# Optimization experiments

Measured on AMD Instinct MI355X. Metric: run time of the kernel, lower is better.

Reference implementation:

```python
import jax, jax.numpy as jnp
import numpy as np

B_, L, DM = 4, 1024, 1024
DI, DS, DR, DC = 1024, 16, 64, 4
NH = 4
DK = DM // NH


def setup_inputs() -> dict:
    key = jax.random.key(0)
    ks = jax.random.split(key, 16)
    def w(i, shape, scale=0.02):
        return jax.random.normal(ks[i], shape, dtype=jnp.float32) * scale
    inp = {
        "x": jax.random.normal(ks[0], (B_, L, DM), dtype=jnp.float32),
        "xx": jax.random.normal(ks[1], (B_, L, DI), dtype=jnp.float32),
        "in_proj_w": w(2, (DI, DM)),
        "conv_w": w(3, (DI, 1, DC)),            # depthwise conv, groups=DI
        "conv_b": jnp.zeros((DI,), jnp.float32),
        "x_proj_w": w(4, (DR + 2 * DS, DI)),
        "dt_proj_w": w(5, (DI, DR)),
        "dt_proj_b": jnp.zeros((DI,), jnp.float32),
        "A_log": jnp.log(jnp.tile(jnp.arange(1, DS + 1, dtype=jnp.float32)[None, :], (DI, 1))),
        "D": jnp.ones((DI,), jnp.float32),
        "wq": w(6, (DM, DM)), "bq": jnp.zeros((DM,), jnp.float32),
        "wk": w(7, (DM, DM)), "bk": jnp.zeros((DM,), jnp.float32),
        "wv": w(8, (DM, DM)), "bv": jnp.zeros((DM,), jnp.float32),
        "wo": w(9, (DM, DM)), "bo": jnp.zeros((DM,), jnp.float32),
    }
    return inp


def _stim_forward(x, xx, in_proj_w, conv_w, conv_b, x_proj_w, dt_proj_w, dt_proj_b,
                  A_log, D, wq, bq, wk, bk, wv, bv, wo, bo):
    b, l, _ = xx.shape
    # query branch: in_proj (Linear, no bias)
    q = x @ in_proj_w.T                                    # (b, l, DI)
    # kv branch: causal depthwise conv1d (padding d_conv-1, truncated to l)
    xc = jnp.transpose(xx, (0, 2, 1))                      # (b, DI, l)
    xc = jax.lax.conv_general_dilated(
        xc, conv_w, window_strides=(1,), padding=[(DC - 1, 0)],
        dimension_numbers=("NCH", "OIH", "NCH"), feature_group_count=DI)
    xc = xc + conv_b[None, :, None]
    u = jax.nn.silu(jnp.transpose(xc, (0, 2, 1)))          # (b, l, DI)
    # SSM parameter projections
    A = -jnp.exp(A_log)                                    # (DI, DS)
    x_dbl = u @ x_proj_w.T                                 # (b, l, DR+2*DS)
    delta, Bm, Cm = jnp.split(x_dbl, [DR, DR + DS], axis=-1)
    delta = jax.nn.softplus(delta @ dt_proj_w.T + dt_proj_b)  # (b, l, DI)
    deltaA = jnp.exp(jnp.einsum("bld,dn->bldn", delta, A))    # (b, l, DI, DS)
    deltaBu = jnp.einsum("bld,bln,bld->bldn", delta, Bm, u)   # (b, l, DI, DS)
    # selective scan over time
    def step(h, inp):
        dA_t, dBu_t, C_t = inp
        h = dA_t * h + dBu_t                               # (b, DI, DS)
        y_t = jnp.einsum("bdn,bn->bd", h, C_t)             # (b, DI)
        return h, y_t
    h0 = jnp.zeros((b, DI, DS), dtype=u.dtype)
    _, ys = jax.lax.scan(step, h0, (jnp.moveaxis(deltaA, 1, 0),
                                    jnp.moveaxis(deltaBu, 1, 0),
                                    jnp.moveaxis(Cm, 1, 0)))
    y = jnp.moveaxis(ys, 0, 1) + u * D                     # (b, l, DI)
    # cross attention: query = q, key/value = y
    Q = (q @ wq.T + bq).reshape(b, l, NH, DK).transpose(0, 2, 1, 3)
    K = (y @ wk.T + bk).reshape(b, l, NH, DK).transpose(0, 2, 1, 3)
    V = (y @ wv.T + bv).reshape(b, l, NH, DK).transpose(0, 2, 1, 3)
    scale = 1.0 / np.sqrt(DK).astype(np.float32)
    scores = jnp.einsum("bhqd,bhkd->bhqk", Q, K) * scale
    attn = jax.nn.softmax(scores, axis=-1)
    out = jnp.einsum("bhqk,bhkd->bhqd", attn, V)
    out = out.transpose(0, 2, 1, 3).reshape(b, l, DM)
    return out @ wo.T + bo


def reference(x, xx, in_proj_w, conv_w, conv_b, x_proj_w, dt_proj_w, dt_proj_b,
              A_log, D, wq, bq, wk, bk, wv, bv, wo, bo):
    return _stim_forward(x, xx, in_proj_w, conv_w, conv_b, x_proj_w, dt_proj_w,
                         dt_proj_b, A_log, D, wq, bq, wk, bk, wv, bv, wo, bo)
```

## Files before the change

kernel.cpp:

```cpp
#include <hip/hip_runtime.h>
#include <math.h>

#define B_  4
#define L_  1024
#define DM  1024
#define DI  1024
#define DS  16
#define DR  64
#define DCV 4
#define NH  4
#define DK  256

#define NCH 32
#define CHL (L_ / NCH)

typedef __attribute__((ext_vector_type(8))) short short8;
typedef __attribute__((ext_vector_type(4))) float floatx4;

static __device__ __forceinline__ unsigned short f2bf(float f) {
    unsigned int u = __float_as_uint(f);
    u += 0x7fffu + ((u >> 16) & 1u);
    return (unsigned short)(u >> 16);
}
static __device__ __forceinline__ float bf2f(unsigned short s) {
    return __uint_as_float(((unsigned int)s) << 16);
}

#define GLL(gp, lp) __builtin_amdgcn_global_load_lds( \
        (const __attribute__((address_space(1))) void*)(gp), \
        (__attribute__((address_space(3))) void*)(lp), 16, 0, 0)

static __device__ __forceinline__ void xcd_rect(int gx, int gy, int& tx, int& ty)
{
    int n = blockIdx.x + gx * blockIdx.y;
    if ((gx & 1) == 0 && (gy & 3) == 0) {
        int xcd = n & 7, j = n >> 3;
        int hx = gx >> 1, qy = gy >> 2;
        tx = (xcd & 1) * hx + (j % hx);
        ty = (xcd >> 1) * qy + (j / hx);
    } else {
        tx = blockIdx.x; ty = blockIdx.y;
    }
}

struct PrepArgs {
    const float* xx; const float* cw; const float* cb;
    unsigned short* ub;
    const float* xs; unsigned short* xd;
    const float* s[6]; unsigned short* d[6];
    int n[6];
    int ns[6];
    const float* tsrc; unsigned short* tdst;
};

__global__ __launch_bounds__(256) void prep(PrepArgs pa)
{
    __shared__ unsigned short tl[32][36];
    int bid = blockIdx.x, tid = threadIdx.x;
    if (bid < 16384) {
        int idx = bid * 256 + tid;
        int d = idx & (DI - 1);
        int l = (idx >> 10) & (L_ - 1);
        int b = idx >> 20;
        const float* xb = pa.xx + (size_t)b * L_ * DI + d;
        float z = pa.cb[d];
#pragma unroll
        for (int j = 0; j < DCV; j++) {
            int t = l - (DCV - 1) + j;
            if (t >= 0) z += xb[(size_t)t * DI] * pa.cw[d * DCV + j];
        }
        float v = z / (1.0f + __expf(-z));
        pa.ub[idx] = f2bf(v);
        return;
    }
    bid -= 16384;
    if (bid < 4096) {
        int i = (bid * 256 + tid) * 4;
        float4 v = *(const float4*)(pa.xs + i);
        ushort4 o;
        o.x = f2bf(v.x); o.y = f2bf(v.y); o.z = f2bf(v.z); o.w = f2bf(v.w);
        *(ushort4*)(pa.xd + i) = o;
        return;
    }
    bid -= 4096;
#pragma unroll
    for (int r = 0; r < 6; r++) {
        int nb = pa.n[r] >> 10;
        if (bid < nb) {
            int i = (bid * 256 + tid) * 4;
            int ns = pa.ns[r];
            const float* s = pa.s[r];
            ushort4 o;
            if (i + 4 <= ns) {
                float4 v = *(const float4*)(s + i);
                o.x = f2bf(v.x); o.y = f2bf(v.y); o.z = f2bf(v.z); o.w = f2bf(v.w);
            } else {
                float v[4];
#pragma unroll
                for (int j = 0; j < 4; j++) v[j] = (i + j < ns) ? s[i + j] : 0.f;
                o.x = f2bf(v[0]); o.y = f2bf(v[1]); o.z = f2bf(v[2]); o.w = f2bf(v[3]);
            }
            *(ushort4*)(pa.d[r] + i) = o;
            return;
        }
        bid -= nb;
    }
    int j0 = (bid >> 5) * 32;
    int n0 = (bid & 31) * 32;
    int r = tid >> 3, c4 = (tid & 7) * 4;
    float4 v = *(const float4*)(pa.tsrc + (size_t)(j0 + r) * 1024 + n0 + c4);
    tl[r][c4 + 0] = f2bf(v.x); tl[r][c4 + 1] = f2bf(v.y);
    tl[r][c4 + 2] = f2bf(v.z); tl[r][c4 + 3] = f2bf(v.w);
    __syncthreads();
    ushort4 o;
    o.x = tl[c4 + 0][r]; o.y = tl[c4 + 1][r];
    o.z = tl[c4 + 2][r]; o.w = tl[c4 + 3][r];
    *(ushort4*)(pa.tdst + (size_t)(n0 + r) * 1024 + j0 + c4) = o;
}

struct GDesc {
    const unsigned short* A;
    const unsigned short* W;
    const float* bias;
    float* Cf;
    unsigned short* Cb;
    int K, lda, ldw, ldc, ldc2;
    int mode;
    float scale;
    int gx, gy;
};
struct GArgs { GDesc g[3]; };

__global__ __launch_bounds__(256) void gemm_multi(GArgs ga)
{
    GDesc g = ga.g[blockIdx.z];
    int bx, by;
    xcd_rect(gridDim.x, gridDim.y, bx, by);
    if (bx >= g.gx || by >= g.gy) return;

    __shared__ __align__(16) unsigned short Asm[3][128 * 32];
    __shared__ __align__(16) unsigned short Bsm[3][128 * 32];

    int tid = threadIdx.x;
    int wid = tid >> 6;
    int lane = tid & 63;
    int wm = wid & 1, wn = wid >> 1;
    int lr = lane & 15, quad = lane >> 4;
    int sq = quad ^ ((lr >> 1) & 3);

    const unsigned short* Ab = g.A + (size_t)by * 128 * g.lda;
    const unsigned short* Wb = g.W + (size_t)bx * 128 * g.ldw;

    int srow = tid >> 2;
    int scol = ((tid & 3) ^ ((tid >> 3) & 3)) * 8;
    const unsigned short* Ap = Ab + (size_t)srow * g.lda + scol;
    const unsigned short* Wp = Wb + (size_t)srow * g.ldw + scol;

    int lbase = (wid * 16) * 32;

    floatx4 acc[4][4];
#pragma unroll
    for (int i = 0; i < 4; i++)
#pragma unroll
        for (int j = 0; j < 4; j++) acc[i][j] = (floatx4){0.f, 0.f, 0.f, 0.f};

#define STAGE_M(buf) do { \
        GLL(Ap, &Asm[buf][lbase]); \
        GLL(Ap + (size_t)64 * g.lda, &Asm[buf][lbase + 64 * 32]); \
        GLL(Wp, &Bsm[buf][lbase]); \
        GLL(Wp + (size_t)64 * g.ldw, &Bsm[buf][lbase + 64 * 32]); \
        Ap += 32; Wp += 32; \
    } while (0)

    int nK = g.K >> 5;
    STAGE_M(0);
    if (nK > 1) STAGE_M(1);

    int cur = 0, stg = 2;
    for (int k = 0; k < nK - 1; k++) {
        asm volatile("s_waitcnt vmcnt(4)" ::: "memory");
        __builtin_amdgcn_s_barrier();
        __builtin_amdgcn_sched_barrier(0);

        short8 af[4], bf[4];
#pragma unroll
        for (int mt = 0; mt < 4; mt++)
            af[mt] = *(const short8*)&Asm[cur][(wm * 64 + mt * 16 + lr) * 32 + sq * 8];
#pragma unroll
        for (int nt = 0; nt < 4; nt++)
            bf[nt] = *(const short8*)&Bsm[cur][(wn * 64 + nt * 16 + lr) * 32 + sq * 8];

        if (k + 2 < nK) {
            STAGE_M(stg);
            stg = (stg == 2) ? 0 : stg + 1;
        }

        __builtin_amdgcn_s_setprio(1);
#pragma unroll
        for (int mt = 0; mt < 4; mt++)
#pragma unroll
            for (int nt = 0; nt < 4; nt++)
                acc[mt][nt] = __builtin_amdgcn_mfma_f32_16x16x32_bf16(
                    af[mt], bf[nt], acc[mt][nt], 0, 0, 0);
        __builtin_amdgcn_s_setprio(0);
        cur = (cur == 2) ? 0 : cur + 1;
    }
    {
        asm volatile("s_waitcnt vmcnt(0)" ::: "memory");
        __builtin_amdgcn_s_barrier();
        __builtin_amdgcn_sched_barrier(0);

        short8 af[4], bf[4];
#pragma unroll
        for (int mt = 0; mt < 4; mt++)
            af[mt] = *(const short8*)&Asm[cur][(wm * 64 + mt * 16 + lr) * 32 + sq * 8];
#pragma unroll
        for (int nt = 0; nt < 4; nt++)
            bf[nt] = *(const short8*)&Bsm[cur][(wn * 64 + nt * 16 + lr) * 32 + sq * 8];
        __builtin_amdgcn_s_setprio(1);
#pragma unroll
        for (int mt = 0; mt < 4; mt++)
#pragma unroll
            for (int nt = 0; nt < 4; nt++)
                acc[mt][nt] = __builtin_amdgcn_mfma_f32_16x16x32_bf16(
                    af[mt], bf[nt], acc[mt][nt], 0, 0, 0);
        __builtin_amdgcn_s_setprio(0);
    }
#undef STAGE_M

    int bm = by * 128, bn = bx * 128;
    int m = g.mode & 3;
#pragma unroll
    for (int mt = 0; mt < 4; mt++) {
#pragma unroll
        for (int nt = 0; nt < 4; nt++) {
            int row0 = bm + wm * 64 + mt * 16 + quad * 4;
            int col = bn + wn * 64 + nt * 16 + lr;
            float bv = g.bias ? g.bias[col] : 0.f;
#pragma unroll
            for (int i = 0; i < 4; i++) {
                float v = acc[mt][nt][i] * g.scale + bv;
                if (g.mode & 4) v = (v > 15.f) ? v : log1pf(__expf(v));
                if (m == 0) {
                    g.Cf[(size_t)(row0 + i) * g.ldc + col] = v;
                } else if (m == 1) {
                    g.Cb[(size_t)(row0 + i) * g.ldc + col] = f2bf(v);
                } else {
                    g.Cf[(size_t)(row0 + i) * g.ldc + col] = v;
                    g.Cb[(size_t)(row0 + i) * g.ldc2 + col] = f2bf(v);
                }
            }
        }
    }
}

__global__ __launch_bounds__(256) void gemm_multi64(GArgs ga)
{
    GDesc g = ga.g[blockIdx.z];
    int bx, by;
    xcd_rect(gridDim.x, gridDim.y, bx, by);
    if (bx >= g.gx || by >= g.gy) return;

    __shared__ __align__(16) unsigned short Asm[3][64 * 32];
    __shared__ __align__(16) unsigned short Bsm[3][128 * 32];

    int tid = threadIdx.x;
    int wid = tid >> 6;
    int lane = tid & 63;
    int wm = wid & 1, wn = wid >> 1;
    int lr = lane & 15, quad = lane >> 4;
    int sq = quad ^ ((lr >> 1) & 3);

    const unsigned short* Ab = g.A + (size_t)by * 64 * g.lda;
    const unsigned short* Wb = g.W + (size_t)bx * 128 * g.ldw;

    int srow = tid >> 2;
    int scol = ((tid & 3) ^ ((tid >> 3) & 3)) * 8;
    const unsigned short* Ap = Ab + (size_t)srow * g.lda + scol;
    const unsigned short* Wp = Wb + (size_t)srow * g.ldw + scol;

    int lbase = (wid * 16) * 32;

    floatx4 acc[2][4];
#pragma unroll
    for (int i = 0; i < 2; i++)
#pragma unroll
        for (int j = 0; j < 4; j++) acc[i][j] = (floatx4){0.f, 0.f, 0.f, 0.f};

#define STAGE_S(buf) do { \
        GLL(Ap, &Asm[buf][lbase]); \
        GLL(Wp, &Bsm[buf][lbase]); \
        GLL(Wp + (size_t)64 * g.ldw, &Bsm[buf][lbase + 64 * 32]); \
        Ap += 32; Wp += 32; \
    } while (0)

    int nK = g.K >> 5;
    STAGE_S(0);
    if (nK > 1) STAGE_S(1);

    int cur = 0, stg = 2;
    for (int k = 0; k < nK - 1; k++) {
        asm volatile("s_waitcnt vmcnt(3)" ::: "memory");
        __builtin_amdgcn_s_barrier();
        __builtin_amdgcn_sched_barrier(0);

        short8 af[2], bf[4];
#pragma unroll
        for (int mt = 0; mt < 2; mt++)
            af[mt] = *(const short8*)&Asm[cur][(wm * 32 + mt * 16 + lr) * 32 + sq * 8];
#pragma unroll
        for (int nt = 0; nt < 4; nt++)
            bf[nt] = *(const short8*)&Bsm[cur][(wn * 64 + nt * 16 + lr) * 32 + sq * 8];

        if (k + 2 < nK) {
            STAGE_S(stg);
            stg = (stg == 2) ? 0 : stg + 1;
        }

        __builtin_amdgcn_s_setprio(1);
#pragma unroll
        for (int mt = 0; mt < 2; mt++)
#pragma unroll
            for (int nt = 0; nt < 4; nt++)
                acc[mt][nt] = __builtin_amdgcn_mfma_f32_16x16x32_bf16(
                    af[mt], bf[nt], acc[mt][nt], 0, 0, 0);
        __builtin_amdgcn_s_setprio(0);
        cur = (cur == 2) ? 0 : cur + 1;
    }
    {
        asm volatile("s_waitcnt vmcnt(0)" ::: "memory");
        __builtin_amdgcn_s_barrier();
        __builtin_amdgcn_sched_barrier(0);

        short8 af[2], bf[4];
#pragma unroll
        for (int mt = 0; mt < 2; mt++)
            af[mt] = *(const short8*)&Asm[cur][(wm * 32 + mt * 16 + lr) * 32 + sq * 8];
#pragma unroll
        for (int nt = 0; nt < 4; nt++)
            bf[nt] = *(const short8*)&Bsm[cur][(wn * 64 + nt * 16 + lr) * 32 + sq * 8];
        __builtin_amdgcn_s_setprio(1);
#pragma unroll
        for (int mt = 0; mt < 2; mt++)
#pragma unroll
            for (int nt = 0; nt < 4; nt++)
                acc[mt][nt] = __builtin_amdgcn_mfma_f32_16x16x32_bf16(
                    af[mt], bf[nt], acc[mt][nt], 0, 0, 0);
        __builtin_amdgcn_s_setprio(0);
    }
#undef STAGE_S

    int bm = by * 64, bn = bx * 128;
    int m = g.mode & 3;
#pragma unroll
    for (int mt = 0; mt < 2; mt++) {
#pragma unroll
        for (int nt = 0; nt < 4; nt++) {
            int row0 = bm + wm * 32 + mt * 16 + quad * 4;
            int col = bn + wn * 64 + nt * 16 + lr;
            float bv = g.bias ? g.bias[col] : 0.f;
#pragma unroll
            for (int i = 0; i < 4; i++) {
                float v = acc[mt][nt][i] * g.scale + bv;
                if (g.mode & 4) v = (v > 15.f) ? v : log1pf(__expf(v));
                if (m == 0) {
                    g.Cf[(size_t)(row0 + i) * g.ldc + col] = v;
                } else if (m == 1) {
                    g.Cb[(size_t)(row0 + i) * g.ldc + col] = f2bf(v);
                } else {
                    g.Cf[(size_t)(row0 + i) * g.ldc + col] = v;
                    g.Cb[(size_t)(row0 + i) * g.ldc2 + col] = f2bf(v);
                }
            }
        }
    }
}

__global__ __launch_bounds__(256) void gemm_batched(
    const unsigned short* __restrict__ A, const unsigned short* __restrict__ W,
    unsigned short* __restrict__ C,
    int K, int lda, int ldw, int ldc,
    long long sA1, long long sA2, long long sW1, long long sW2,
    long long sC1, long long sC2, float scale)
{
    __shared__ __align__(16) unsigned short Asm[3][128 * 32];
    __shared__ __align__(16) unsigned short Bsm[3][128 * 32];

    int bx, by;
    xcd_rect(gridDim.x, gridDim.y, bx, by);

    int z = blockIdx.z;
    long long bq = z >> 2, hq = z & 3;
    int tid = threadIdx.x;
    int wid = tid >> 6;
    int lane = tid & 63;
    int wm = wid & 1, wn = wid >> 1;
    int lr = lane & 15, quad = lane >> 4;
    int sq = quad ^ ((lr >> 1) & 3);

    const unsigned short* Ab = A + bq * sA1 + hq * sA2 + (size_t)by * 128 * lda;
    const unsigned short* Wb = W + bq * sW1 + hq * sW2 + (size_t)bx * 128 * ldw;

    int srow = tid >> 2;
    int scol = ((tid & 3) ^ ((tid >> 3) & 3)) * 8;
    const unsigned short* Ap = Ab + (size_t)srow * lda + scol;
    const unsigned short* Wp = Wb + (size_t)srow * ldw + scol;

    int lbase = (wid * 16) * 32;

    floatx4 acc[4][4];
#pragma unroll
    for (int i = 0; i < 4; i++)
#pragma unroll
        for (int j = 0; j < 4; j++) acc[i][j] = (floatx4){0.f, 0.f, 0.f, 0.f};

#define STAGE_B(buf) do { \
        GLL(Ap, &Asm[buf][lbase]); \
        GLL(Ap + (size_t)64 * lda, &Asm[buf][lbase + 64 * 32]); \
        GLL(Wp, &Bsm[buf][lbase]); \
        GLL(Wp + (size_t)64 * ldw, &Bsm[buf][lbase + 64 * 32]); \
        Ap += 32; Wp += 32; \
    } while (0)

    int nK = K >> 5;
    STAGE_B(0);
    if (nK > 1) STAGE_B(1);

    int cur = 0, stg = 2;
    for (int k = 0; k < nK - 1; k++) {
        asm volatile("s_waitcnt vmcnt(4)" ::: "memory");
        __builtin_amdgcn_s_barrier();
        __builtin_amdgcn_sched_barrier(0);

        short8 af[4], bf[4];
#pragma unroll
        for (int mt = 0; mt < 4; mt++)
            af[mt] = *(const short8*)&Asm[cur][(wm * 64 + mt * 16 + lr) * 32 + sq * 8];
#pragma unroll
        for (int nt = 0; nt < 4; nt++)
            bf[nt] = *(const short8*)&Bsm[cur][(wn * 64 + nt * 16 + lr) * 32 + sq * 8];

        if (k + 2 < nK) {
            STAGE_B(stg);
            stg = (stg == 2) ? 0 : stg + 1;
        }

        __builtin_amdgcn_s_setprio(1);
#pragma unroll
        for (int mt = 0; mt < 4; mt++)
#pragma unroll
            for (int nt = 0; nt < 4; nt++)
                acc[mt][nt] = __builtin_amdgcn_mfma_f32_16x16x32_bf16(
                    af[mt], bf[nt], acc[mt][nt], 0, 0, 0);
        __builtin_amdgcn_s_setprio(0);
        cur = (cur == 2) ? 0 : cur + 1;
    }
    {
        asm volatile("s_waitcnt vmcnt(0)" ::: "memory");
        __builtin_amdgcn_s_barrier();
        __builtin_amdgcn_sched_barrier(0);

        short8 af[4], bf[4];
#pragma unroll
        for (int mt = 0; mt < 4; mt++)
            af[mt] = *(const short8*)&Asm[cur][(wm * 64 + mt * 16 + lr) * 32 + sq * 8];
#pragma unroll
        for (int nt = 0; nt < 4; nt++)
            bf[nt] = *(const short8*)&Bsm[cur][(wn * 64 + nt * 16 + lr) * 32 + sq * 8];
        __builtin_amdgcn_s_setprio(1);
#pragma unroll
        for (int mt = 0; mt < 4; mt++)
#pragma unroll
            for (int nt = 0; nt < 4; nt++)
                acc[mt][nt] = __builtin_amdgcn_mfma_f32_16x16x32_bf16(
                    af[mt], bf[nt], acc[mt][nt], 0, 0, 0);
        __builtin_amdgcn_s_setprio(0);
    }
#undef STAGE_B

    long long coff = bq * sC1 + hq * sC2;
    int bm = by * 128, bn = bx * 128;
    unsigned short* Cb = C + coff;

#pragma unroll
    for (int mt = 0; mt < 4; mt++) {
#pragma unroll
        for (int nt = 0; nt < 4; nt++) {
            int row0 = bm + wm * 64 + mt * 16 + quad * 4;
            int col = bn + wn * 64 + nt * 16 + lr;
#pragma unroll
            for (int i = 0; i < 4; i++)
                Cb[(size_t)(row0 + i) * ldc + col] = f2bf(acc[mt][nt][i] * scale);
        }
    }
}

__global__ __launch_bounds__(256) void gemm_batched64(
    const unsigned short* __restrict__ A, const unsigned short* __restrict__ W,
    unsigned short* __restrict__ C,
    int K, int lda, int ldw, int ldc,
    long long sA1, long long sA2, long long sW1, long long sW2,
    long long sC1, long long sC2, float scale)
{
    __shared__ __align__(16) unsigned short Asm[3][64 * 32];
    __shared__ __align__(16) unsigned short Bsm[3][128 * 32];

    int bx, by;
    xcd_rect(gridDim.x, gridDim.y, bx, by);

    int z = blockIdx.z;
    long long bq = z >> 2, hq = z & 3;
    int tid = threadIdx.x;
    int wid = tid >> 6;
    int lane = tid & 63;
    int wm = wid & 1, wn = wid >> 1;
    int lr = lane & 15, quad = lane >> 4;
    int sq = quad ^ ((lr >> 1) & 3);

    const unsigned short* Ab = A + bq * sA1 + hq * sA2 + (size_t)by * 64 * lda;
    const unsigned short* Wb = W + bq * sW1 + hq * sW2 + (size_t)bx * 128 * ldw;

    int srow = tid >> 2;
    int scol = ((tid & 3) ^ ((tid >> 3) & 3)) * 8;
    const unsigned short* Ap = Ab + (size_t)srow * lda + scol;
    const unsigned short* Wp = Wb + (size_t)srow * ldw + scol;

    int lbase = (wid * 16) * 32;

    floatx4 acc[2][4];
#pragma unroll
    for (int i = 0; i < 2; i++)
#pragma unroll
        for (int j = 0; j < 4; j++) acc[i][j] = (floatx4){0.f, 0.f, 0.f, 0.f};

#define STAGE_S(buf) do { \
        GLL(Ap, &Asm[buf][lbase]); \
        GLL(Wp, &Bsm[buf][lbase]); \
        GLL(Wp + (size_t)64 * ldw, &Bsm[buf][lbase + 64 * 32]); \
        Ap += 32; Wp += 32; \
    } while (0)

    int nK = K >> 5;
    STAGE_S(0);
    if (nK > 1) STAGE_S(1);

    int cur = 0, stg = 2;
    for (int k = 0; k < nK - 1; k++) {
        asm volatile("s_waitcnt vmcnt(3)" ::: "memory");
        __builtin_amdgcn_s_barrier();
        __builtin_amdgcn_sched_barrier(0);

        short8 af[2], bf[4];
#pragma unroll
        for (int mt = 0; mt < 2; mt++)
            af[mt] = *(const short8*)&Asm[cur][(wm * 32 + mt * 16 + lr) * 32 + sq * 8];
#pragma unroll
        for (int nt = 0; nt < 4; nt++)
            bf[nt] = *(const short8*)&Bsm[cur][(wn * 64 + nt * 16 + lr) * 32 + sq * 8];

        if (k + 2 < nK) {
            STAGE_S(stg);
            stg = (stg == 2) ? 0 : stg + 1;
        }

        __builtin_amdgcn_s_setprio(1);
#pragma unroll
        for (int mt = 0; mt < 2; mt++)
#pragma unroll
            for (int nt = 0; nt < 4; nt++)
                acc[mt][nt] = __builtin_amdgcn_mfma_f32_16x16x32_bf16(
                    af[mt], bf[nt], acc[mt][nt], 0, 0, 0);
        __builtin_amdgcn_s_setprio(0);
        cur = (cur == 2) ? 0 : cur + 1;
    }
    {
        asm volatile("s_waitcnt vmcnt(0)" ::: "memory");
        __builtin_amdgcn_s_barrier();
        __builtin_amdgcn_sched_barrier(0);

        short8 af[2], bf[4];
#pragma unroll
        for (int mt = 0; mt < 2; mt++)
            af[mt] = *(const short8*)&Asm[cur][(wm * 32 + mt * 16 + lr) * 32 + sq * 8];
#pragma unroll
        for (int nt = 0; nt < 4; nt++)
            bf[nt] = *(const short8*)&Bsm[cur][(wn * 64 + nt * 16 + lr) * 32 + sq * 8];
        __builtin_amdgcn_s_setprio(1);
#pragma unroll
        for (int mt = 0; mt < 2; mt++)
#pragma unroll
            for (int nt = 0; nt < 4; nt++)
                acc[mt][nt] = __builtin_amdgcn_mfma_f32_16x16x32_bf16(
                    af[mt], bf[nt], acc[mt][nt], 0, 0, 0);
        __builtin_amdgcn_s_setprio(0);
    }
#undef STAGE_S

    long long coff = bq * sC1 + hq * sC2;
    int bm = by * 64, bn = bx * 128;
    unsigned short* Cb = C + coff;

#pragma unroll
    for (int mt = 0; mt < 2; mt++) {
#pragma unroll
        for (int nt = 0; nt < 4; nt++) {
            int row0 = bm + wm * 32 + mt * 16 + quad * 4;
            int col = bn + wn * 64 + nt * 16 + lr;
#pragma unroll
            for (int i = 0; i < 4; i++)
                Cb[(size_t)(row0 + i) * ldc + col] = f2bf(acc[mt][nt][i] * scale);
        }
    }
}

__global__ __launch_bounds__(256) void scan_a(
    const float* __restrict__ delta, const unsigned short* __restrict__ u,
    const float* __restrict__ xdbl, const float* __restrict__ A_log,
    float* __restrict__ Hc, float* __restrict__ sumdv)
{
    int gid = blockIdx.x * 256 + threadIdx.x;
    int c = gid >> 12;
    int bd = gid & 4095;
    int b = bd >> 10, d = bd & 1023;

    float a[16];
#pragma unroll
    for (int j = 0; j < 4; j++) {
        float4 al = *(const float4*)(A_log + d * 16 + j * 4);
        a[j * 4 + 0] = -__expf(al.x); a[j * 4 + 1] = -__expf(al.y);
        a[j * 4 + 2] = -__expf(al.z); a[j * 4 + 3] = -__expf(al.w);
    }
    float h[16];
#pragma unroll
    for (int n = 0; n < 16; n++) h[n] = 0.f;
    float sd = 0.f;

    int t0 = c * CHL;
    const float* dp = delta + ((size_t)(b * L_) + t0) * DI + d;
    const unsigned short* up = u + ((size_t)(b * L_) + t0) * DI + d;
    const float* xp = xdbl + ((size_t)(b * L_) + t0) * 128;

#pragma unroll 4
    for (int t = 0; t < CHL; t++) {
        float dv = dp[t * DI];
        float uv = bf2f(up[t * DI]);
        float duv = dv * uv;
        sd += dv;
        float Bv[16];
#pragma unroll
        for (int j = 0; j < 4; j++) {
            float4 bq = *(const float4*)(xp + t * 128 + 64 + j * 4);
            Bv[j * 4 + 0] = bq.x; Bv[j * 4 + 1] = bq.y;
            Bv[j * 4 + 2] = bq.z; Bv[j * 4 + 3] = bq.w;
        }
#pragma unroll
        for (int n = 0; n < 16; n++)
            h[n] = __expf(dv * a[n]) * h[n] + duv * Bv[n];
    }

    float* hp = Hc + ((size_t)c * 4096 + bd) * 16;
#pragma unroll
    for (int j = 0; j < 4; j++)
        *(float4*)(hp + j * 4) = make_float4(h[j * 4], h[j * 4 + 1], h[j * 4 + 2], h[j * 4 + 3]);
    sumdv[c * 4096 + bd] = sd;
}

__global__ __launch_bounds__(256) void scan_b(
    float* __restrict__ Hc, const float* __restrict__ sumdv,
    const float* __restrict__ A_log)
{
    int bd = blockIdx.x * 256 + threadIdx.x;
    int d = bd & 1023;

    float a[16];
#pragma unroll
    for (int j = 0; j < 4; j++) {
        float4 al = *(const float4*)(A_log + d * 16 + j * 4);
        a[j * 4 + 0] = -__expf(al.x); a[j * 4 + 1] = -__expf(al.y);
        a[j * 4 + 2] = -__expf(al.z); a[j * 4 + 3] = -__expf(al.w);
    }
    float H[16];
#pragma unroll
    for (int n = 0; n < 16; n++) H[n] = 0.f;

    for (int c = 0; c < NCH; c++) {
        float* hp = Hc + ((size_t)c * 4096 + bd) * 16;
        float sdv = sumdv[c * 4096 + bd];
        float hc[16];
#pragma unroll
        for (int j = 0; j < 4; j++) {
            float4 q = *(const float4*)(hp + j * 4);
            hc[j * 4 + 0] = q.x; hc[j * 4 + 1] = q.y; hc[j * 4 + 2] = q.z; hc[j * 4 + 3] = q.w;
        }
#pragma unroll
        for (int j = 0; j < 4; j++)
            *(float4*)(hp + j * 4) = make_float4(H[j * 4], H[j * 4 + 1], H[j * 4 + 2], H[j * 4 + 3]);
#pragma unroll
        for (int n = 0; n < 16; n++)
            H[n] = __expf(a[n] * sdv) * H[n] + hc[n];
    }
}

__global__ __launch_bounds__(256) void scan_c(
    const float* __restrict__ delta, const unsigned short* __restrict__ u,
    const float* __restrict__ xdbl, const float* __restrict__ A_log,
    const float* __restrict__ Dv, const float* __restrict__ Hstart,
    unsigned short* __restrict__ y)
{
    int gid = blockIdx.x * 256 + threadIdx.x;
    int c = gid >> 12;
    int bd = gid & 4095;
    int b = bd >> 10, d = bd & 1023;

    float a[16];
#pragma unroll
    for (int j = 0; j < 4; j++) {
        float4 al = *(const float4*)(A_log + d * 16 + j * 4);
        a[j * 4 + 0] = -__expf(al.x); a[j * 4 + 1] = -__expf(al.y);
        a[j * 4 + 2] = -__expf(al.z); a[j * 4 + 3] = -__expf(al.w);
    }
    float h[16];
    const float* hp = Hstart + ((size_t)c * 4096 + bd) * 16;
#pragma unroll
    for (int j = 0; j < 4; j++) {
        float4 q = *(const float4*)(hp + j * 4);
        h[j * 4 + 0] = q.x; h[j * 4 + 1] = q.y; h[j * 4 + 2] = q.z; h[j * 4 + 3] = q.w;
    }
    float Dd = Dv[d];

    int t0 = c * CHL;
    const float* dp = delta + ((size_t)(b * L_) + t0) * DI + d;
    const unsigned short* up = u + ((size_t)(b * L_) + t0) * DI + d;
    const float* xp = xdbl + ((size_t)(b * L_) + t0) * 128;
    unsigned short* yp = y + ((size_t)(b * L_) + t0) * DI + d;

#pragma unroll 4
    for (int t = 0; t < CHL; t++) {
        float dv = dp[t * DI];
        float uv = bf2f(up[t * DI]);
        float duv = dv * uv;
        float Bv[16], Cv[16];
#pragma unroll
        for (int j = 0; j < 4; j++) {
            float4 bq = *(const float4*)(xp + t * 128 + 64 + j * 4);
            Bv[j * 4 + 0] = bq.x; Bv[j * 4 + 1] = bq.y;
            Bv[j * 4 + 2] = bq.z; Bv[j * 4 + 3] = bq.w;
            float4 cq = *(const float4*)(xp + t * 128 + 80 + j * 4);
            Cv[j * 4 + 0] = cq.x; Cv[j * 4 + 1] = cq.y;
            Cv[j * 4 + 2] = cq.z; Cv[j * 4 + 3] = cq.w;
        }
        float ys = 0.f;
#pragma unroll
        for (int n = 0; n < 16; n++) {
            h[n] = __expf(dv * a[n]) * h[n] + duv * Bv[n];
            ys += h[n] * Cv[n];
        }
        yp[t * DI] = f2bf(ys + uv * Dd);
    }
}

__global__ __launch_bounds__(256) void softmax_transpose(
    unsigned short* __restrict__ S,
    const unsigned short* __restrict__ V, unsigned short* __restrict__ VT)
{
    __shared__ unsigned short tl[32][36];
    int bid = blockIdx.x;
    if (bid < 4096) {
        int row = bid * 4 + (threadIdx.x >> 6);
        int lane = threadIdx.x & 63;
        unsigned short* p = S + (size_t)row * 1024;

        float v[16];
#pragma unroll
        for (int ch = 0; ch < 4; ch++) {
            ushort4 u4 = *(const ushort4*)(p + ch * 256 + lane * 4);
            v[ch * 4 + 0] = bf2f(u4.x); v[ch * 4 + 1] = bf2f(u4.y);
            v[ch * 4 + 2] = bf2f(u4.z); v[ch * 4 + 3] = bf2f(u4.w);
        }
        float m = -1e30f;
#pragma unroll
        for (int i = 0; i < 16; i++) m = fmaxf(m, v[i]);
#pragma unroll
        for (int off = 32; off >= 1; off >>= 1) m = fmaxf(m, __shfl_xor(m, off));
        float s = 0.f;
#pragma unroll
        for (int i = 0; i < 16; i++) { v[i] = __expf(v[i] - m); s += v[i]; }
#pragma unroll
        for (int off = 32; off >= 1; off >>= 1) s += __shfl_xor(s, off);
        float inv = 1.0f / s;
#pragma unroll
        for (int ch = 0; ch < 4; ch++) {
            ushort4 o;
            o.x = f2bf(v[ch * 4 + 0] * inv); o.y = f2bf(v[ch * 4 + 1] * inv);
            o.z = f2bf(v[ch * 4 + 2] * inv); o.w = f2bf(v[ch * 4 + 3] * inv);
            *(ushort4*)(p + ch * 256 + lane * 4) = o;
        }
        return;
    }
    int tb = bid - 4096;
    int bh = tb >> 8;
    int rem = tb & 255;
    int d0 = (rem >> 5) * 32;
    int l0 = (rem & 31) * 32;
    int b = bh >> 2, h = bh & 3;
    int tid = threadIdx.x;
    int r = tid >> 3, c4 = (tid & 7) * 4;

    const unsigned short* src = V + ((size_t)(b * L_ + l0 + r)) * 1024 + h * DK + d0 + c4;
    ushort4 v = *(const ushort4*)src;
    tl[r][c4 + 0] = v.x; tl[r][c4 + 1] = v.y; tl[r][c4 + 2] = v.z; tl[r][c4 + 3] = v.w;
    __syncthreads();

    unsigned short* dst = VT + ((size_t)bh * DK + d0 + r) * L_ + l0 + c4;
    ushort4 o;
    o.x = tl[c4 + 0][r]; o.y = tl[c4 + 1][r]; o.z = tl[c4 + 2][r]; o.w = tl[c4 + 3][r];
    *(ushort4*)dst = o;
}

extern "C" void kernel_launch(void* const* d_in, const int* in_sizes, int n_in,
                              void* d_out, int out_size, void* d_ws, size_t ws_size,
                              hipStream_t stream)
{
    const float* x         = (const float*)d_in[0];
    const float* xx        = (const float*)d_in[1];
    const float* in_proj_w = (const float*)d_in[2];
    const float* conv_w    = (const float*)d_in[3];
    const float* conv_b    = (const float*)d_in[4];
    const float* x_proj_w  = (const float*)d_in[5];
    const float* dt_proj_w = (const float*)d_in[6];
    const float* dt_proj_b = (const float*)d_in[7];
    const float* A_log     = (const float*)d_in[8];
    const float* Dvec      = (const float*)d_in[9];
    const float* wq        = (const float*)d_in[10];
    const float* bq        = (const float*)d_in[11];
    const float* wk        = (const float*)d_in[12];
    const float* bk        = (const float*)d_in[13];
    const float* wv        = (const float*)d_in[14];
    const float* bv        = (const float*)d_in[15];
    const float* wo        = (const float*)d_in[16];
    const float* bo        = (const float*)d_in[17];
    float* out = (float*)d_out;

    char* w = (char*)d_ws;
    const size_t MB = 1024 * 1024, KB = 1024;
    float*          Hc     = (float*)(w + 0);
    float*          delta  = (float*)(w + 16 * MB);
    unsigned short* Sbuf   = (unsigned short*)(w + 0);
    unsigned short* x_bf   = (unsigned short*)(w + 32 * MB);
    unsigned short* Q_bf   = (unsigned short*)(w + 40 * MB);
    unsigned short* VT     = Q_bf;
    unsigned short* y_bf   = (unsigned short*)(w + 48 * MB);
    unsigned short* AO     = y_bf;
    unsigned short* K_bf   = (unsigned short*)(w + 56 * MB);
    unsigned short* V_bf   = (unsigned short*)(w + 64 * MB);
    unsigned short* u_bf   = (unsigned short*)(w + 72 * MB);
    float*          xdbl   = (float*)(w + 80 * MB);
    unsigned short* xdblb  = (unsigned short*)(w + 82 * MB);
    unsigned short* w_inT  = (unsigned short*)(w + 83 * MB);
    unsigned short* w_q    = (unsigned short*)(w + 85 * MB);
    unsigned short* w_k    = (unsigned short*)(w + 87 * MB);
    unsigned short* w_v    = (unsigned short*)(w + 89 * MB);
    unsigned short* w_o    = (unsigned short*)(w + 91 * MB);
    unsigned short* w_xp   = (unsigned short*)(w + 93 * MB);
    unsigned short* w_dt   = (unsigned short*)(w + 93 * MB + 256 * KB);
    float*          sumdv  = (float*)(w + 93 * MB + 384 * KB);
    unsigned short* W_qin  = (unsigned short*)(w + 95 * MB);

    dim3 blk(256);
    const long long LL = L_;

    PrepArgs pa;
    pa.xx = xx; pa.cw = conv_w; pa.cb = conv_b; pa.ub = u_bf;
    pa.xs = x; pa.xd = x_bf;
    pa.s[0] = wq;        pa.d[0] = w_q;  pa.n[0] = 1048576; pa.ns[0] = 1048576;
    pa.s[1] = wk;        pa.d[1] = w_k;  pa.n[1] = 1048576; pa.ns[1] = 1048576;
    pa.s[2] = wv;        pa.d[2] = w_v;  pa.n[2] = 1048576; pa.ns[2] = 1048576;
    pa.s[3] = wo;        pa.d[3] = w_o;  pa.n[3] = 1048576; pa.ns[3] = 1048576;
    pa.s[4] = x_proj_w;  pa.d[4] = w_xp; pa.n[4] = 131072;  pa.ns[4] = 98304;
    pa.s[5] = dt_proj_w; pa.d[5] = w_dt; pa.n[5] = 65536;   pa.ns[5] = 65536;
    pa.tsrc = in_proj_w; pa.tdst = w_inT;
    prep<<<dim3(25792), blk, 0, stream>>>(pa);

    {
        GArgs ga = {};
        ga.g[0] = (GDesc){w_q, w_inT, nullptr, nullptr, W_qin,
                          1024, 1024, 1024, 1024, 0, 1, 1.0f, 8, 16};
        ga.g[1] = (GDesc){u_bf, w_xp, nullptr, xdbl, xdblb,
                          1024, 1024, 1024, 128, 128, 2, 1.0f, 1, 64};
        gemm_multi64<<<dim3(8, 64, 2), blk, 0, stream>>>(ga);
    }
    {
        GArgs ga = {};
        ga.g[0] = (GDesc){xdblb, w_dt, dt_proj_b, delta, nullptr,
                          64, 128, 64, 1024, 0, 0 | 4, 1.0f, 8, 64};
        gemm_multi64<<<dim3(8, 64, 1), blk, 0, stream>>>(ga);
    }
    scan_a<<<dim3(512), blk, 0, stream>>>(delta, u_bf, xdbl, A_log, Hc, sumdv);
    scan_b<<<dim3(16), blk, 0, stream>>>(Hc, sumdv, A_log);
    scan_c<<<dim3(512), blk, 0, stream>>>(delta, u_bf, xdbl, A_log, Dvec, Hc, y_bf);

    {
        GArgs ga = {};
        ga.g[0] = (GDesc){x_bf, W_qin, bq, nullptr, Q_bf, 1024, 1024, 1024, 1024, 0, 1, 1.0f, 8, 32};
        ga.g[1] = (GDesc){y_bf, w_k, bk, nullptr, K_bf, 1024, 1024, 1024, 1024, 0, 1, 1.0f, 8, 32};
        ga.g[2] = (GDesc){y_bf, w_v, bv, nullptr, V_bf, 1024, 1024, 1024, 1024, 0, 1, 1.0f, 8, 32};
        gemm_multi<<<dim3(8, 32, 3), blk, 0, stream>>>(ga);
    }
    gemm_batched<<<dim3(8, 8, 16), blk, 0, stream>>>(Q_bf, K_bf, Sbuf,
        DK, 1024, 1024, 1024,
        LL * 1024, 256, LL * 1024, 256,
        4 * LL * 1024, LL * 1024, 0.0625f);
    softmax_transpose<<<dim3(8192), blk, 0, stream>>>(Sbuf, V_bf, VT);
    gemm_batched64<<<dim3(2, 16, 16), blk, 0, stream>>>(Sbuf, VT, AO,
        1024, 1024, 1024, 1024,
        4 * LL * 1024, LL * 1024,
        4 * (long long)DK * 1024, (long long)DK * 1024,
        LL * 1024, 256, 1.0f);
    {
        GArgs ga = {};
        ga.g[0] = (GDesc){AO, w_o, bo, out, nullptr, 1024, 1024, 1024, 1024, 0, 0, 1.0f, 8, 64};
        gemm_multi64<<<dim3(8, 64, 1), blk, 0, stream>>>(ga);
    }
}
```

Measured before the change: 388.1 us.

## Fuse softmax into PV GEMM prologue and A-fragment load path

Removes the standalone softmax pass over the score matrix. Each PV GEMM block now computes its rows' max and sum-of-exp in a prologue by reading the 64 score rows directly, then applies exp and normalization to the A fragments right before the MFMAs. The V transpose becomes its own kernel. This saves a full read-write of the 16M-element score buffer, but every PV block redundantly rereads its score rows (two grid columns share them), and exp work is added inside the MFMA loop.

```diff
diff --git a/kernel.cpp b/kernel.cpp
--- a/kernel.cpp
+++ b/kernel.cpp
@@ -495,7 +495,7 @@
     }
 }
 
-__global__ __launch_bounds__(256) void gemm_batched64(
+__global__ __launch_bounds__(256) void gemm_pv64(
     const unsigned short* __restrict__ A, const unsigned short* __restrict__ W,
     unsigned short* __restrict__ C,
     int K, int lda, int ldw, int ldc,
@@ -520,6 +520,42 @@
     const unsigned short* Ab = A + bq * sA1 + hq * sA2 + (size_t)by * 64 * lda;
     const unsigned short* Wb = W + bq * sW1 + hq * sW2 + (size_t)bx * 128 * ldw;
 
+    float* scr = (float*)&Asm[0][0];
+    {
+        int r = tid & 63, seg = tid >> 6;
+        const unsigned short* Sr = Ab + (size_t)r * lda + seg * 256;
+        float mt = -1e30f;
+#pragma unroll 8
+        for (int i = 0; i < 32; i++) {
+            short8 v = *(const short8*)(Sr + i * 8);
+#pragma unroll
+            for (int e = 0; e < 8; e++) mt = fmaxf(mt, bf2f((unsigned short)v[e]));
+        }
+        float st = 0.f;
+#pragma unroll 8
+        for (int i = 0; i < 32; i++) {
+            short8 v = *(const short8*)(Sr + i * 8);
+#pragma unroll
+            for (int e = 0; e < 8; e++) st += __expf(bf2f((unsigned short)v[e]) - mt);
+        }
+        scr[seg * 64 + r] = mt;
+        scr[256 + seg * 64 + r] = st;
+    }
+    __syncthreads();
+    if (tid < 64) {
+        float m0 = scr[tid], m1 = scr[64 + tid], m2 = scr[128 + tid], m3 = scr[192 + tid];
+        float mm = fmaxf(fmaxf(m0, m1), fmaxf(m2, m3));
+        float ss = scr[256 + tid] * __expf(m0 - mm) + scr[320 + tid] * __expf(m1 - mm)
+                 + scr[384 + tid] * __expf(m2 - mm) + scr[448 + tid] * __expf(m3 - mm);
+        scr[512 + tid] = mm;
+        scr[576 + tid] = 1.0f / ss;
+    }
+    __syncthreads();
+    int r0 = wm * 32 + lr, r1 = r0 + 16;
+    float mA0 = scr[512 + r0], iv0 = scr[576 + r0];
+    float mA1 = scr[512 + r1], iv1 = scr[576 + r1];
+    __syncthreads();
+
     int srow = tid >> 2;
     int scol = ((tid & 3) ^ ((tid >> 3) & 3)) * 8;
     const unsigned short* Ap = Ab + (size_t)srow * lda + scol;
@@ -533,16 +569,22 @@
 #pragma unroll
         for (int j = 0; j < 4; j++) acc[i][j] = (floatx4){0.f, 0.f, 0.f, 0.f};
 
-#define STAGE_S(buf) do { \
+#define STAGE_P(buf) do { \
         GLL(Ap, &Asm[buf][lbase]); \
         GLL(Wp, &Bsm[buf][lbase]); \
         GLL(Wp + (size_t)64 * ldw, &Bsm[buf][lbase + 64 * 32]); \
         Ap += 32; Wp += 32; \
     } while (0)
 
+#define SOFTEN(af_, mA_, iv_) do { \
+_Pragma("unroll") \
+        for (int e = 0; e < 8; e++) \
+            af_[e] = (short)f2bf(__expf(bf2f((unsigned short)af_[e]) - mA_) * iv_); \
+    } while (0)
+
     int nK = K >> 5;
-    STAGE_S(0);
-    if (nK > 1) STAGE_S(1);
+    STAGE_P(0);
+    if (nK > 1) STAGE_P(1);
 
     int cur = 0, stg = 2;
     for (int k = 0; k < nK - 1; k++) {
@@ -550,26 +592,30 @@
         __builtin_amdgcn_s_barrier();
         __builtin_amdgcn_sched_barrier(0);
 
-        short8 af[2], bf[4];
-#pragma unroll
-        for (int mt = 0; mt < 2; mt++)
-            af[mt] = *(const short8*)&Asm[cur][(wm * 32 + mt * 16 + lr) * 32 + sq * 8];
+        short8 af0, af1, bf[4];
+        af0 = *(const short8*)&Asm[cur][(wm * 32 + lr) * 32 + sq * 8];
+        af1 = *(const short8*)&Asm[cur][(wm * 32 + 16 + lr) * 32 + sq * 8];
 #pragma unroll
         for (int nt = 0; nt < 4; nt++)
             bf[nt] = *(const short8*)&Bsm[cur][(wn * 64 + nt * 16 + lr) * 32 + sq * 8];
 
         if (k + 2 < nK) {
-            STAGE_S(stg);
+            STAGE_P(stg);
             stg = (stg == 2) ? 0 : stg + 1;
         }
 
+        SOFTEN(af0, mA0, iv0);
+        SOFTEN(af1, mA1, iv1);
+
         __builtin_amdgcn_s_setprio(1);
 #pragma unroll
-        for (int mt = 0; mt < 2; mt++)
-#pragma unroll
-            for (int nt = 0; nt < 4; nt++)
-                acc[mt][nt] = __builtin_amdgcn_mfma_f32_16x16x32_bf16(
-                    af[mt], bf[nt], acc[mt][nt], 0, 0, 0);
+        for (int nt = 0; nt < 4; nt++)
+            acc[0][nt] = __builtin_amdgcn_mfma_f32_16x16x32_bf16(
+                af0, bf[nt], acc[0][nt], 0, 0, 0);
+#pragma unroll
+        for (int nt = 0; nt < 4; nt++)
+            acc[1][nt] = __builtin_amdgcn_mfma_f32_16x16x32_bf16(
+                af1, bf[nt], acc[1][nt], 0, 0, 0);
         __builtin_amdgcn_s_setprio(0);
         cur = (cur == 2) ? 0 : cur + 1;
     }
@@ -578,23 +624,27 @@
         __builtin_amdgcn_s_barrier();
         __builtin_amdgcn_sched_barrier(0);
 
-        short8 af[2], bf[4];
-#pragma unroll
-        for (int mt = 0; mt < 2; mt++)
-            af[mt] = *(const short8*)&Asm[cur][(wm * 32 + mt * 16 + lr) * 32 + sq * 8];
+        short8 af0, af1, bf[4];
+        af0 = *(const short8*)&Asm[cur][(wm * 32 + lr) * 32 + sq * 8];
+        af1 = *(const short8*)&Asm[cur][(wm * 32 + 16 + lr) * 32 + sq * 8];
 #pragma unroll
         for (int nt = 0; nt < 4; nt++)
             bf[nt] = *(const short8*)&Bsm[cur][(wn * 64 + nt * 16 + lr) * 32 + sq * 8];
+        SOFTEN(af0, mA0, iv0);
+        SOFTEN(af1, mA1, iv1);
         __builtin_amdgcn_s_setprio(1);
 #pragma unroll
-        for (int mt = 0; mt < 2; mt++)
-#pragma unroll
-            for (int nt = 0; nt < 4; nt++)
-                acc[mt][nt] = __builtin_amdgcn_mfma_f32_16x16x32_bf16(
-                    af[mt], bf[nt], acc[mt][nt], 0, 0, 0);
+        for (int nt = 0; nt < 4; nt++)
+            acc[0][nt] = __builtin_amdgcn_mfma_f32_16x16x32_bf16(
+                af0, bf[nt], acc[0][nt], 0, 0, 0);
+#pragma unroll
+        for (int nt = 0; nt < 4; nt++)
+            acc[1][nt] = __builtin_amdgcn_mfma_f32_16x16x32_bf16(
+                af1, bf[nt], acc[1][nt], 0, 0, 0);
         __builtin_amdgcn_s_setprio(0);
     }
-#undef STAGE_S
+#undef STAGE_P
+#undef SOFTEN
 
     long long coff = bq * sC1 + hq * sC2;
     int bm = by * 64, bn = bx * 128;
@@ -759,50 +809,13 @@
     }
 }
 
-__global__ __launch_bounds__(256) void softmax_transpose(
-    unsigned short* __restrict__ S,
+__global__ __launch_bounds__(256) void transpose_v(
     const unsigned short* __restrict__ V, unsigned short* __restrict__ VT)
 {
     __shared__ unsigned short tl[32][36];
-    int bid = blockIdx.x;
-    if (bid < 4096) {
-        int row = bid * 4 + (threadIdx.x >> 6);
-        int lane = threadIdx.x & 63;
-        unsigned short* p = S + (size_t)row * 1024;
-
-        float v[16];
-#pragma unroll
-        for (int ch = 0; ch < 4; ch++) {
-            ushort4 u4 = *(const ushort4*)(p + ch * 256 + lane * 4);
-            v[ch * 4 + 0] = bf2f(u4.x); v[ch * 4 + 1] = bf2f(u4.y);
-            v[ch * 4 + 2] = bf2f(u4.z); v[ch * 4 + 3] = bf2f(u4.w);
-        }
-        float m = -1e30f;
-#pragma unroll
-        for (int i = 0; i < 16; i++) m = fmaxf(m, v[i]);
-#pragma unroll
-        for (int off = 32; off >= 1; off >>= 1) m = fmaxf(m, __shfl_xor(m, off));
-        float s = 0.f;
-#pragma unroll
-        for (int i = 0; i < 16; i++) { v[i] = __expf(v[i] - m); s += v[i]; }
-#pragma unroll
-        for (int off = 32; off >= 1; off >>= 1) s += __shfl_xor(s, off);
-        float inv = 1.0f / s;
-#pragma unroll
-        for (int ch = 0; ch < 4; ch++) {
-            ushort4 o;
-            o.x = f2bf(v[ch * 4 + 0] * inv); o.y = f2bf(v[ch * 4 + 1] * inv);
-            o.z = f2bf(v[ch * 4 + 2] * inv); o.w = f2bf(v[ch * 4 + 3] * inv);
-            *(ushort4*)(p + ch * 256 + lane * 4) = o;
-        }
-        return;
-    }
-    int tb = bid - 4096;
-    int bh = tb >> 8;
-    int rem = tb & 255;
-    int d0 = (rem >> 5) * 32;
-    int l0 = (rem & 31) * 32;
+    int bh = blockIdx.z;
     int b = bh >> 2, h = bh & 3;
+    int l0 = blockIdx.x * 32, d0 = blockIdx.y * 32;
     int tid = threadIdx.x;
     int r = tid >> 3, c4 = (tid & 7) * 4;
 
@@ -910,8 +923,8 @@
         DK, 1024, 1024, 1024,
         LL * 1024, 256, LL * 1024, 256,
         4 * LL * 1024, LL * 1024, 0.0625f);
-    softmax_transpose<<<dim3(8192), blk, 0, stream>>>(Sbuf, V_bf, VT);
-    gemm_batched64<<<dim3(2, 16, 16), blk, 0, stream>>>(Sbuf, VT, AO,
+    transpose_v<<<dim3(32, 8, 16), blk, 0, stream>>>(V_bf, VT);
+    gemm_pv64<<<dim3(2, 16, 16), blk, 0, stream>>>(Sbuf, VT, AO,
         1024, 1024, 1024, 1024,
         4 * LL * 1024, LL * 1024,
         4 * (long long)DK * 1024, (long long)DK * 1024,
```

Result: slower. 402.0 us (+3.6%).
